# Kernel optimization log

Measured on AMD Instinct MI355X. Metric: run time of the kernel, lower is better.

The kernel has to match this reference:

```python
import jax, jax.numpy as jnp
import numpy as np

N = 50000      # nodes
E = 800000     # edges
CIN = 128
CH = 128
COUT = 64
EPS = 1e-5     # BatchNorm eps


def setup_inputs() -> dict:
    key = jax.random.key(0)
    ks = jax.random.split(key, 16)
    s = 0.1  # weight scale for numerical stability
    return {
        "x": jax.random.normal(ks[0], (N, CIN), jnp.float32),
        "edge_index": jax.random.randint(ks[1], (2, E), 0, N, jnp.int32),
        "edge_weights": jax.random.uniform(ks[2], (E,), jnp.float32),
        "w1": jax.random.normal(ks[3], (CIN, CH), jnp.float32) * s,
        "b1": jnp.zeros((CH,), jnp.float32),
        "bn1_g": jnp.ones((CH,), jnp.float32),
        "bn1_b": jnp.zeros((CH,), jnp.float32),
        "bn1_m": jax.random.normal(ks[4], (CH,), jnp.float32) * 0.1,
        "bn1_v": jax.random.uniform(ks[5], (CH,), jnp.float32) + 0.5,
        "conv_ws": jax.random.normal(ks[6], (2, CH, CH), jnp.float32) * s,
        "conv_bs": jnp.zeros((2, CH), jnp.float32),
        "bns_g": jnp.ones((2, CH), jnp.float32),
        "bns_b": jnp.zeros((2, CH), jnp.float32),
        "bns_m": jax.random.normal(ks[7], (2, CH), jnp.float32) * 0.1,
        "bns_v": jax.random.uniform(ks[8], (2, CH), jnp.float32) + 0.5,
        "lin1_w": jax.random.normal(ks[9], (CH, CH), jnp.float32) * s,
        "lin1_b": jnp.zeros((CH,), jnp.float32),
        "lin2_w": jax.random.normal(ks[10], (CH, COUT), jnp.float32) * s,
        "lin2_b": jnp.zeros((COUT,), jnp.float32),
    }


def _bn(h, g, b, m, v):
    # BatchNorm1d in eval mode: running statistics
    return (h - m) * jax.lax.rsqrt(v + EPS) * g + b


def _gcn(h, w, b, src, dst, norm, n):
    # GCNConv: out[dst] += norm_e * (h @ W)[src]  (self loops already in src/dst)
    h = h @ w
    msg = h[src] * norm[:, None]                 # [E+N, CH]
    return jax.ops.segment_sum(msg, dst, num_segments=n) + b


def reference(x, edge_index, edge_weights, w1, b1, bn1_g, bn1_b, bn1_m, bn1_v,
              conv_ws, conv_bs, bns_g, bns_b, bns_m, bns_v,
              lin1_w, lin1_b, lin2_w, lin2_b):
    n = x.shape[0]
    loop = jnp.arange(n, dtype=edge_index.dtype)
    src = jnp.concatenate([edge_index[0], loop])
    dst = jnp.concatenate([edge_index[1], loop])
    ew = jnp.concatenate([edge_weights, jnp.ones((n,), edge_weights.dtype)])
    # symmetric degree normalization (PyG gcn_norm)
    deg = jax.ops.segment_sum(ew, dst, num_segments=n)
    dis = jnp.where(deg > 0, jax.lax.rsqrt(deg), 0.0)
    norm = dis[src] * ew * dis[dst]

    lrelu = jax.nn.leaky_relu  # slope 0.01, matches F.leaky_relu default
    h = lrelu(_bn(_gcn(x, w1, b1, src, dst, norm, n), bn1_g, bn1_b, bn1_m, bn1_v))
    for i in range(conv_ws.shape[0]):
        h = lrelu(_bn(_gcn(h, conv_ws[i], conv_bs[i], src, dst, norm, n),
                      bns_g[i], bns_b[i], bns_m[i], bns_v[i]) + h)
    h = lrelu(h @ lin1_w + lin1_b)
    # dropout is identity in eval mode
    return h @ lin2_w + lin2_b
```

## Files before the change

kernel.cpp:

```cpp
#include <hip/hip_runtime.h>
#include <hip/hip_bf16.h>


constexpr int   NN    = 50000;
constexpr int   EE    = 800000;
constexpr int   CH    = 128;
constexpr int   SLOTS = 64;
constexpr int   NBUK  = 782;
constexpr int   RCAP  = 2048;
constexpr int   EPB   = 4096;
constexpr float EPS   = 1e-5f;

typedef __attribute__((ext_vector_type(8))) short bf16x8;
typedef __attribute__((ext_vector_type(4))) float f32x4;
typedef unsigned long long u64;
typedef unsigned short u16;

__device__ inline u16 f2bf_rne(float f) {
  unsigned u = __float_as_uint(f);
  unsigned r = u + 0x7fffu + ((u >> 16) & 1u);
  return (u16)(r >> 16);
}
__device__ inline float bf2f(unsigned h16) {
  return __uint_as_float(h16 << 16);
}


__global__ __launch_bounds__(256) void bin_kernel(const int* __restrict__ ei,
                                                  const float* __restrict__ ew,
                                                  unsigned* __restrict__ gcur,
                                                  u64* __restrict__ bins) {
  __shared__ unsigned cnt[NBUK];
  __shared__ unsigned base[NBUK];
  const int tid = threadIdx.x;
  for (int b = tid; b < NBUK; b += 256) cnt[b] = 0;
  __syncthreads();
  const int e0 = blockIdx.x * EPB;
  unsigned pk[16]; u16 bkt[16]; u16 rnk[16]; unsigned char dl[16];
  #pragma unroll
  for (int i = 0; i < 16; i++) {
    int e = e0 + i * 256 + tid;
    if (e < EE) {
      int s = ei[e], d = ei[EE + e];
      float w = ew[e];
      bkt[i] = (u16)(d >> 6);
      dl[i]  = (unsigned char)(d & 63);
      pk[i]  = ((unsigned)f2bf_rne(w) << 16) | (unsigned)s;
      rnk[i] = (u16)atomicAdd(&cnt[bkt[i]], 1u);
    } else bkt[i] = 0xffffu;
  }
  __syncthreads();
  for (int b = tid; b < NBUK; b += 256) {
    unsigned c = cnt[b];
    base[b] = c ? atomicAdd(&gcur[b * 16], c) : 0u;
  }
  __syncthreads();
  #pragma unroll
  for (int i = 0; i < 16; i++) {
    if (bkt[i] == 0xffffu) continue;
    unsigned pos = base[bkt[i]] + rnk[i];
    if (pos < RCAP)
      bins[(size_t)bkt[i] * RCAP + pos] = ((u64)dl[i] << 32) | pk[i];
  }
}


__global__ __launch_bounds__(256) void scatter_kernel(const unsigned* __restrict__ gcur,
                                                      const u64* __restrict__ bins,
                                                      unsigned* __restrict__ ell,
                                                      float* __restrict__ dis) {
  __shared__ unsigned rank[64];
  __shared__ float    wsum[64];
  const int b   = blockIdx.x;
  const int tid = threadIdx.x;
  if (tid < 64) { rank[tid] = 1u; wsum[tid] = 0.f; }
  __syncthreads();
  unsigned cnt = gcur[b * 16];
  if (cnt > RCAP) cnt = RCAP;
  const u64* src = bins + (size_t)b * RCAP;
  for (unsigned i = tid; i < cnt; i += 256) {
    u64 v = src[i];
    unsigned pk = (unsigned)v;
    unsigned dl = (unsigned)(v >> 32);
    unsigned r = atomicAdd(&rank[dl], 1u);
    if (r < SLOTS)
      ell[((size_t)(b * 64 + dl)) * SLOTS + r] = pk;
    atomicAdd(&wsum[dl], bf2f(pk >> 16));
  }
  __syncthreads();
  if (tid < 64) {
    int node = b * 64 + tid;
    if (node < NN) {
      unsigned c = rank[tid];
      if (c > SLOTS) c = SLOTS;
      ell[(size_t)node * SLOTS] = c;
      dis[node] = rsqrtf(1.0f + wsum[tid]);
    }
  }
}

constexpr int NB_WZ = (73728 + 384 + 255) / 256;

__global__ void wswz_kernel(
    const float* __restrict__ w1, const float* __restrict__ bn1_g, const float* __restrict__ bn1_v,
    const float* __restrict__ conv_ws, const float* __restrict__ bns_g, const float* __restrict__ bns_v,
    const float* __restrict__ lin1_w, const float* __restrict__ lin2_w,
    const float* __restrict__ b1, const float* __restrict__ bn1_b, const float* __restrict__ bn1_m,
    const float* __restrict__ conv_bs, const float* __restrict__ bns_b, const float* __restrict__ bns_m,
    u16* __restrict__ w1h, u16* __restrict__ w1l,
    u16* __restrict__ c0h, u16* __restrict__ c0l,
    u16* __restrict__ c1h, u16* __restrict__ c1l,
    u16* __restrict__ l1h, u16* __restrict__ l1l,
    u16* __restrict__ l2h, u16* __restrict__ l2l,
    float* __restrict__ beff)
{
  int idx = blockIdx.x * 256 + threadIdx.x;
  if (idx >= 73728) {
    int r = idx - 73728;
    if (r >= 384) return;
    int l = r >> 7, c = r & 127;
    float bc, gg, bb, mm, vv;
    if (l == 0) { bc = b1[c]; gg = bn1_g[c]; bb = bn1_b[c]; mm = bn1_m[c]; vv = bn1_v[c]; }
    else {
      int o = (l - 1) * 128 + c;
      bc = conv_bs[o]; gg = bns_g[o]; bb = bns_b[o]; mm = bns_m[o]; vv = bns_v[o];
    }
    beff[r] = (bc - mm) * gg * rsqrtf(vv + EPS) + bb;
    return;
  }
  const float* W; const float* g = nullptr; const float* v = nullptr;
  u16 *hi, *lo; int CO = 128; int local;
  if      (idx < 16384) { W = w1;              g = bn1_g;     v = bn1_v;     hi = w1h; lo = w1l; local = idx; }
  else if (idx < 32768) { W = conv_ws;         g = bns_g;     v = bns_v;     hi = c0h; lo = c0l; local = idx - 16384; }
  else if (idx < 49152) { W = conv_ws + 16384; g = bns_g+128; v = bns_v+128; hi = c1h; lo = c1l; local = idx - 32768; }
  else if (idx < 65536) { W = lin1_w;                                        hi = l1h; lo = l1l; local = idx - 49152; }
  else                  { W = lin2_w;                                        hi = l2h; lo = l2l; local = idx - 65536; CO = 64; }
  int k = local / CO, n = local % CO;
  float w = W[local];
  if (g) w *= g[n] * rsqrtf(v[n] + EPS);
  int NCT = CO / 16;
  int kchunk = k >> 5, kin = k & 31, quad = kin >> 3, j = kin & 7;
  int ct = n >> 4, l = (quad << 4) | (n & 15);
  size_t pos = ((size_t)(kchunk * NCT + ct) * 64 + l) * 8 + j;
  u16 h = f2bf_rne(w);
  hi[pos] = h;
  lo[pos] = f2bf_rne(w - bf2f(h));
}

template<int CO, int EPI, bool OUT_BF16, bool A_BF16, bool SCALE>
__global__ __launch_bounds__(256) void mgemm_kernel(
    const void* __restrict__ Ain,
    const u16* __restrict__ Whi, const u16* __restrict__ Wlo,
    const float* __restrict__ bias, const float* __restrict__ dis,
    void* __restrict__ Cout)
{
  constexpr int NCT = CO / 16;
  __shared__ float lds[64][CO + 4];

  const int tid  = threadIdx.x;
  const int wave = tid >> 6;
  const int lane = tid & 63;
  const int quad = lane >> 4;
  const int mrow = lane & 15;
  const int row0 = blockIdx.x * 64;

  int arow = row0 + wave * 16 + mrow;
  if (arow >= NN) arow = NN - 1;

  bf16x8 ahi[4], alo[4];
  if constexpr (A_BF16) {
    const u16* Ar = (const u16*)Ain + (size_t)arow * CH;
    #pragma unroll
    for (int c = 0; c < 4; c++)
      ahi[c] = *(const bf16x8*)(Ar + c * 32 + quad * 8);
  } else {
    const float* Ar = (const float*)Ain + (size_t)arow * CH;
    #pragma unroll
    for (int c = 0; c < 4; c++) {
      int off = c * 32 + quad * 8;
      float4 f0 = *(const float4*)(Ar + off);
      float4 f1 = *(const float4*)(Ar + off + 4);
      float f[8] = {f0.x, f0.y, f0.z, f0.w, f1.x, f1.y, f1.z, f1.w};
      #pragma unroll
      for (int j = 0; j < 8; j++) {
        u16 h = f2bf_rne(f[j]);
        ahi[c][j] = (short)h;
        alo[c][j] = (short)f2bf_rne(f[j] - bf2f(h));
      }
    }
  }

  f32x4 acc[NCT];
  #pragma unroll
  for (int t = 0; t < NCT; t++) acc[t] = (f32x4){0.f, 0.f, 0.f, 0.f};

  #pragma unroll
  for (int c = 0; c < 4; c++) {
    #pragma unroll
    for (int t = 0; t < NCT; t++) {
      size_t base = ((size_t)(c * NCT + t) * 64 + lane) * 8;
      bf16x8 bh = *(const bf16x8*)(Whi + base);
      bf16x8 bl = *(const bf16x8*)(Wlo + base);
      acc[t] = __builtin_amdgcn_mfma_f32_16x16x32_bf16(ahi[c], bh, acc[t], 0, 0, 0);
      if constexpr (!A_BF16)
        acc[t] = __builtin_amdgcn_mfma_f32_16x16x32_bf16(alo[c], bh, acc[t], 0, 0, 0);
      acc[t] = __builtin_amdgcn_mfma_f32_16x16x32_bf16(ahi[c], bl, acc[t], 0, 0, 0);
    }
  }

  #pragma unroll
  for (int t = 0; t < NCT; t++)
    #pragma unroll
    for (int r = 0; r < 4; r++)
      lds[wave * 16 + quad * 4 + r][t * 16 + mrow] = acc[t][r];
  __syncthreads();

  constexpr int TOTE = 64 * CO / 4;
  #pragma unroll
  for (int i = tid; i < TOTE; i += 256) {
    int row = (i * 4) / CO;
    int col = (i * 4) % CO;
    int grow = row0 + row;
    if (grow >= NN) continue;
    float rs = 1.0f;
    if constexpr (SCALE) rs = dis[grow];
    const float* lp = &lds[row][col];
    float o[4];
    #pragma unroll
    for (int q = 0; q < 4; q++) {
      float x = lp[q];
      if constexpr (EPI >= 1) {
        x += bias[col + q];
        if constexpr (EPI == 1) x = x > 0.f ? x : 0.01f * x;
      }
      if constexpr (SCALE) x *= rs;
      o[q] = x;
    }
    if constexpr (OUT_BF16) {
      u16* cp = (u16*)Cout + (size_t)grow * CO + col;
      unsigned p0 = ((unsigned)f2bf_rne(o[1]) << 16) | f2bf_rne(o[0]);
      unsigned p1 = ((unsigned)f2bf_rne(o[3]) << 16) | f2bf_rne(o[2]);
      *(uint2*)cp = make_uint2(p0, p1);
    } else {
      float* cp = (float*)Cout + (size_t)grow * CO + col;
      *(float4*)cp = make_float4(o[0], o[1], o[2], o[3]);
    }
  }
}

__global__ __launch_bounds__(256) void linf_kernel(
    const u16* __restrict__ Ain,
    const u16* __restrict__ l1h, const u16* __restrict__ l1l,
    const float* __restrict__ b1,
    const u16* __restrict__ l2h, const u16* __restrict__ l2l,
    const float* __restrict__ b2, float* __restrict__ out)
{
  __shared__ float lds[64][CH + 4];
  const int tid  = threadIdx.x;
  const int wave = tid >> 6;
  const int lane = tid & 63;
  const int quad = lane >> 4;
  const int mrow = lane & 15;
  const int row0 = blockIdx.x * 64;

  int arow = row0 + wave * 16 + mrow;
  if (arow >= NN) arow = NN - 1;

  bf16x8 a1[4];
  {
    const u16* Ar = Ain + (size_t)arow * CH;
    #pragma unroll
    for (int c = 0; c < 4; c++)
      a1[c] = *(const bf16x8*)(Ar + c * 32 + quad * 8);
  }
  f32x4 acc[8];
  #pragma unroll
  for (int t = 0; t < 8; t++) acc[t] = (f32x4){0.f, 0.f, 0.f, 0.f};
  #pragma unroll
  for (int c = 0; c < 4; c++) {
    #pragma unroll
    for (int t = 0; t < 8; t++) {
      size_t base = ((size_t)(c * 8 + t) * 64 + lane) * 8;
      bf16x8 bh = *(const bf16x8*)(l1h + base);
      bf16x8 bl = *(const bf16x8*)(l1l + base);
      acc[t] = __builtin_amdgcn_mfma_f32_16x16x32_bf16(a1[c], bh, acc[t], 0, 0, 0);
      acc[t] = __builtin_amdgcn_mfma_f32_16x16x32_bf16(a1[c], bl, acc[t], 0, 0, 0);
    }
  }
  #pragma unroll
  for (int t = 0; t < 8; t++) {
    float bb = b1[t * 16 + mrow];
    #pragma unroll
    for (int r = 0; r < 4; r++) {
      float x = acc[t][r] + bb;
      x = x > 0.f ? x : 0.01f * x;
      lds[wave * 16 + quad * 4 + r][t * 16 + mrow] = x;
    }
  }
  __syncthreads();

  f32x4 acc2[4];
  #pragma unroll
  for (int t = 0; t < 4; t++) acc2[t] = (f32x4){0.f, 0.f, 0.f, 0.f};
  const int lrow = wave * 16 + mrow;
  #pragma unroll
  for (int c = 0; c < 4; c++) {
    bf16x8 ahi, alo;
    const float* lp = &lds[lrow][c * 32 + quad * 8];
    float4 f0 = *(const float4*)lp;
    float4 f1 = *(const float4*)(lp + 4);
    float f[8] = {f0.x, f0.y, f0.z, f0.w, f1.x, f1.y, f1.z, f1.w};
    #pragma unroll
    for (int j = 0; j < 8; j++) {
      u16 h = f2bf_rne(f[j]);
      ahi[j] = (short)h;
      alo[j] = (short)f2bf_rne(f[j] - bf2f(h));
    }
    #pragma unroll
    for (int t = 0; t < 4; t++) {
      size_t base = ((size_t)(c * 4 + t) * 64 + lane) * 8;
      bf16x8 bh = *(const bf16x8*)(l2h + base);
      bf16x8 bl = *(const bf16x8*)(l2l + base);
      acc2[t] = __builtin_amdgcn_mfma_f32_16x16x32_bf16(ahi, bh, acc2[t], 0, 0, 0);
      acc2[t] = __builtin_amdgcn_mfma_f32_16x16x32_bf16(alo, bh, acc2[t], 0, 0, 0);
      acc2[t] = __builtin_amdgcn_mfma_f32_16x16x32_bf16(ahi, bl, acc2[t], 0, 0, 0);
    }
  }
  #pragma unroll
  for (int t = 0; t < 4; t++) {
    float bb = b2[t * 16 + mrow];
    #pragma unroll
    for (int r = 0; r < 4; r++) {
      int grow = row0 + wave * 16 + quad * 4 + r;
      if (grow < NN)
        out[(size_t)grow * 64 + t * 16 + mrow] = acc2[t][r] + bb;
    }
  }
}

template<bool RES>
__global__ __launch_bounds__(256) void agg_kernel(
    const u16* __restrict__ hw,
    const unsigned* __restrict__ ell, const float* __restrict__ dis,
    const float* __restrict__ beff,
    const u16* __restrict__ res, u16* __restrict__ out)
{
  int node = (blockIdx.x * blockDim.x + threadIdx.x) >> 6;
  int lane = threadIdx.x & 63;
  if (node >= NN) return;
  const int sub = lane & 15;
  const int grp = lane >> 4;

  unsigned myword = ell[(size_t)node * SLOTS + lane];
  int cnt = __shfl((int)myword, 0);
  if (cnt > SLOTS) cnt = SLOTS;

  float a[8] = {0.f, 0.f, 0.f, 0.f, 0.f, 0.f, 0.f, 0.f};

  for (int j = 0; j < cnt; j += 8) {
    int j0 = j + grp, j1 = j + 4 + grp;
    unsigned e0 = (unsigned)__shfl((int)myword, j0);
    unsigned e1 = (unsigned)__shfl((int)myword, j1 & 63);
    float    w0 = (j0 == 0) ? 1.0f : bf2f(e0 >> 16);
    unsigned s0 = (j0 == 0) ? (unsigned)node : (e0 & 0xffffu);
    float    w1 = bf2f(e1 >> 16);
    unsigned s1 = e1 & 0xffffu;
    if (j0 >= cnt) { w0 = 0.f; s0 = (unsigned)node; }
    if (j1 >= cnt) { w1 = 0.f; s1 = (unsigned)node; }
    uint4 h0 = *(const uint4*)(hw + (size_t)s0 * CH + sub * 8);
    uint4 h1 = *(const uint4*)(hw + (size_t)s1 * CH + sub * 8);
    a[0] = fmaf(w0, bf2f(h0.x & 0xffffu), a[0]); a[1] = fmaf(w0, bf2f(h0.x >> 16), a[1]);
    a[2] = fmaf(w0, bf2f(h0.y & 0xffffu), a[2]); a[3] = fmaf(w0, bf2f(h0.y >> 16), a[3]);
    a[4] = fmaf(w0, bf2f(h0.z & 0xffffu), a[4]); a[5] = fmaf(w0, bf2f(h0.z >> 16), a[5]);
    a[6] = fmaf(w0, bf2f(h0.w & 0xffffu), a[6]); a[7] = fmaf(w0, bf2f(h0.w >> 16), a[7]);
    a[0] = fmaf(w1, bf2f(h1.x & 0xffffu), a[0]); a[1] = fmaf(w1, bf2f(h1.x >> 16), a[1]);
    a[2] = fmaf(w1, bf2f(h1.y & 0xffffu), a[2]); a[3] = fmaf(w1, bf2f(h1.y >> 16), a[3]);
    a[4] = fmaf(w1, bf2f(h1.z & 0xffffu), a[4]); a[5] = fmaf(w1, bf2f(h1.z >> 16), a[5]);
    a[6] = fmaf(w1, bf2f(h1.w & 0xffffu), a[6]); a[7] = fmaf(w1, bf2f(h1.w >> 16), a[7]);
  }

  #pragma unroll
  for (int k = 0; k < 8; k++) {
    a[k] += __shfl_xor(a[k], 16);
    a[k] += __shfl_xor(a[k], 32);
  }

  if (grp == 0) {
    float disd = dis[node];
    int c = sub * 8;
    float4 be0 = *(const float4*)(beff + c);
    float4 be1 = *(const float4*)(beff + c + 4);
    float y[8];
    y[0] = a[0] * disd + be0.x; y[1] = a[1] * disd + be0.y;
    y[2] = a[2] * disd + be0.z; y[3] = a[3] * disd + be0.w;
    y[4] = a[4] * disd + be1.x; y[5] = a[5] * disd + be1.y;
    y[6] = a[6] * disd + be1.z; y[7] = a[7] * disd + be1.w;
    if constexpr (RES) {
      uint4 r = *(const uint4*)(res + (size_t)node * CH + c);
      y[0] += bf2f(r.x & 0xffffu); y[1] += bf2f(r.x >> 16);
      y[2] += bf2f(r.y & 0xffffu); y[3] += bf2f(r.y >> 16);
      y[4] += bf2f(r.z & 0xffffu); y[5] += bf2f(r.z >> 16);
      y[6] += bf2f(r.w & 0xffffu); y[7] += bf2f(r.w >> 16);
    }
    #pragma unroll
    for (int k = 0; k < 8; k++) y[k] = y[k] > 0.f ? y[k] : 0.01f * y[k];
    uint4 o;
    o.x = ((unsigned)f2bf_rne(y[1]) << 16) | f2bf_rne(y[0]);
    o.y = ((unsigned)f2bf_rne(y[3]) << 16) | f2bf_rne(y[2]);
    o.z = ((unsigned)f2bf_rne(y[5]) << 16) | f2bf_rne(y[4]);
    o.w = ((unsigned)f2bf_rne(y[7]) << 16) | f2bf_rne(y[6]);
    *(uint4*)(out + (size_t)node * CH + c) = o;
  }
}


extern "C" void kernel_launch(void* const* d_in, const int* in_sizes, int n_in,
                              void* d_out, int out_size, void* d_ws, size_t ws_size,
                              hipStream_t stream) {
  const float* x       = (const float*)d_in[0];
  const int*   ei      = (const int*)  d_in[1];
  const float* ew      = (const float*)d_in[2];
  const float* w1      = (const float*)d_in[3];
  const float* b1      = (const float*)d_in[4];
  const float* bn1_g   = (const float*)d_in[5];
  const float* bn1_b   = (const float*)d_in[6];
  const float* bn1_m   = (const float*)d_in[7];
  const float* bn1_v   = (const float*)d_in[8];
  const float* conv_ws = (const float*)d_in[9];
  const float* conv_bs = (const float*)d_in[10];
  const float* bns_g   = (const float*)d_in[11];
  const float* bns_b   = (const float*)d_in[12];
  const float* bns_m   = (const float*)d_in[13];
  const float* bns_v   = (const float*)d_in[14];
  const float* lin1_w  = (const float*)d_in[15];
  const float* lin1_b  = (const float*)d_in[16];
  const float* lin2_w  = (const float*)d_in[17];
  const float* lin2_b  = (const float*)d_in[18];
  float* out = (float*)d_out;

  size_t off = 0;
  auto alloc = [&](size_t elems) -> void* {
    void* p = (char*)d_ws + off * 4;
    off += (elems + 3) & ~(size_t)3;
    return p;
  };
  unsigned* gcur = (unsigned*)alloc(NBUK * 16);
  u64*      bins = (u64*)     alloc((size_t)NBUK * RCAP * 2);
  unsigned* ell  = (unsigned*)alloc((size_t)NN * SLOTS);
  float*    dis  = (float*)   alloc(NN);
  float*    beff = (float*)   alloc(3 * CH);
  u16*      hwb  = (u16*)     alloc((size_t)NN * CH / 2);
  u16*      hA   = (u16*)     alloc((size_t)NN * CH / 2);
  u16* w1h = (u16*)alloc(CH * CH / 2); u16* w1l = (u16*)alloc(CH * CH / 2);
  u16* c0h = (u16*)alloc(CH * CH / 2); u16* c0l = (u16*)alloc(CH * CH / 2);
  u16* c1h = (u16*)alloc(CH * CH / 2); u16* c1l = (u16*)alloc(CH * CH / 2);
  u16* l1h = (u16*)alloc(CH * CH / 2); u16* l1l = (u16*)alloc(CH * CH / 2);
  u16* l2h = (u16*)alloc(CH * 64 / 2); u16* l2l = (u16*)alloc(CH * 64 / 2);

  const int nb_bin  = (EE + EPB - 1) / EPB;
  const int nb_gemm = (NN + 63) / 64;
  const int nb_agg  = (NN * 64 + 255) / 256;
  dim3 B(256);

  hipMemsetAsync(gcur, 0, NBUK * 16 * sizeof(unsigned), stream);
  bin_kernel    <<<nb_bin, B, 0, stream>>>(ei, ew, gcur, bins);
  scatter_kernel<<<NBUK,   B, 0, stream>>>(gcur, bins, ell, dis);

  wswz_kernel<<<NB_WZ, B, 0, stream>>>(w1, bn1_g, bn1_v, conv_ws, bns_g, bns_v,
      lin1_w, lin2_w, b1, bn1_b, bn1_m, conv_bs, bns_b, bns_m,
      w1h, w1l, c0h, c0l, c1h, c1l, l1h, l1l, l2h, l2l, beff);

  mgemm_kernel<128, 0, true, false, true><<<nb_gemm, B, 0, stream>>>(x, w1h, w1l, nullptr, dis, hwb);
  agg_kernel<false><<<nb_agg, B, 0, stream>>>(hwb, ell, dis, beff, nullptr, hA);

  mgemm_kernel<128, 0, true, true, true><<<nb_gemm, B, 0, stream>>>(hA, c0h, c0l, nullptr, dis, hwb);
  agg_kernel<true><<<nb_agg, B, 0, stream>>>(hwb, ell, dis, beff + CH, hA, hA);

  mgemm_kernel<128, 0, true, true, true><<<nb_gemm, B, 0, stream>>>(hA, c1h, c1l, nullptr, dis, hwb);
  agg_kernel<true><<<nb_agg, B, 0, stream>>>(hwb, ell, dis, beff + 2 * CH, hA, hA);

  linf_kernel<<<nb_gemm, B, 0, stream>>>(hA, l1h, l1l, lin1_b, l2h, l2l, lin2_b, out);
}
```

Before: 324.3 us.

## Fuse GCN aggregation with the following layer's GEMM per 64-node block

```diff
diff --git a/kernel.cpp b/kernel.cpp
--- a/kernel.cpp
+++ b/kernel.cpp
@@ -147,16 +147,12 @@
   lo[pos] = f2bf_rne(w - bf2f(h));
 }
 
-template<int CO, int EPI, bool OUT_BF16, bool A_BF16, bool SCALE>
-__global__ __launch_bounds__(256) void mgemm_kernel(
-    const void* __restrict__ Ain,
+__global__ __launch_bounds__(256) void gemm1_kernel(
+    const float* __restrict__ Ain,
     const u16* __restrict__ Whi, const u16* __restrict__ Wlo,
-    const float* __restrict__ bias, const float* __restrict__ dis,
-    void* __restrict__ Cout)
+    const float* __restrict__ dis, u16* __restrict__ Cout)
 {
-  constexpr int NCT = CO / 16;
-  __shared__ float lds[64][CO + 4];
-
+  __shared__ float lds[64][CH + 4];
   const int tid  = threadIdx.x;
   const int wave = tid >> 6;
   const int lane = tid & 63;
@@ -168,88 +164,195 @@
   if (arow >= NN) arow = NN - 1;
 
   bf16x8 ahi[4], alo[4];
-  if constexpr (A_BF16) {
-    const u16* Ar = (const u16*)Ain + (size_t)arow * CH;
-    #pragma unroll
-    for (int c = 0; c < 4; c++)
-      ahi[c] = *(const bf16x8*)(Ar + c * 32 + quad * 8);
-  } else {
-    const float* Ar = (const float*)Ain + (size_t)arow * CH;
-    #pragma unroll
-    for (int c = 0; c < 4; c++) {
-      int off = c * 32 + quad * 8;
-      float4 f0 = *(const float4*)(Ar + off);
-      float4 f1 = *(const float4*)(Ar + off + 4);
-      float f[8] = {f0.x, f0.y, f0.z, f0.w, f1.x, f1.y, f1.z, f1.w};
-      #pragma unroll
-      for (int j = 0; j < 8; j++) {
-        u16 h = f2bf_rne(f[j]);
-        ahi[c][j] = (short)h;
-        alo[c][j] = (short)f2bf_rne(f[j] - bf2f(h));
-      }
-    }
-  }
-
-  f32x4 acc[NCT];
-  #pragma unroll
-  for (int t = 0; t < NCT; t++) acc[t] = (f32x4){0.f, 0.f, 0.f, 0.f};
-
+  const float* Ar = Ain + (size_t)arow * CH;
   #pragma unroll
   for (int c = 0; c < 4; c++) {
-    #pragma unroll
-    for (int t = 0; t < NCT; t++) {
-      size_t base = ((size_t)(c * NCT + t) * 64 + lane) * 8;
+    int off = c * 32 + quad * 8;
+    float4 f0 = *(const float4*)(Ar + off);
+    float4 f1 = *(const float4*)(Ar + off + 4);
+    float f[8] = {f0.x, f0.y, f0.z, f0.w, f1.x, f1.y, f1.z, f1.w};
+    #pragma unroll
+    for (int j = 0; j < 8; j++) {
+      u16 h = f2bf_rne(f[j]);
+      ahi[c][j] = (short)h;
+      alo[c][j] = (short)f2bf_rne(f[j] - bf2f(h));
+    }
+  }
+
+  f32x4 acc[8];
+  #pragma unroll
+  for (int t = 0; t < 8; t++) acc[t] = (f32x4){0.f, 0.f, 0.f, 0.f};
+  #pragma unroll
+  for (int c = 0; c < 4; c++) {
+    #pragma unroll
+    for (int t = 0; t < 8; t++) {
+      size_t base = ((size_t)(c * 8 + t) * 64 + lane) * 8;
       bf16x8 bh = *(const bf16x8*)(Whi + base);
       bf16x8 bl = *(const bf16x8*)(Wlo + base);
       acc[t] = __builtin_amdgcn_mfma_f32_16x16x32_bf16(ahi[c], bh, acc[t], 0, 0, 0);
-      if constexpr (!A_BF16)
-        acc[t] = __builtin_amdgcn_mfma_f32_16x16x32_bf16(alo[c], bh, acc[t], 0, 0, 0);
+      acc[t] = __builtin_amdgcn_mfma_f32_16x16x32_bf16(alo[c], bh, acc[t], 0, 0, 0);
       acc[t] = __builtin_amdgcn_mfma_f32_16x16x32_bf16(ahi[c], bl, acc[t], 0, 0, 0);
     }
   }
 
   #pragma unroll
-  for (int t = 0; t < NCT; t++)
+  for (int t = 0; t < 8; t++)
     #pragma unroll
     for (int r = 0; r < 4; r++)
       lds[wave * 16 + quad * 4 + r][t * 16 + mrow] = acc[t][r];
   __syncthreads();
 
-  constexpr int TOTE = 64 * CO / 4;
-  #pragma unroll
-  for (int i = tid; i < TOTE; i += 256) {
-    int row = (i * 4) / CO;
-    int col = (i * 4) % CO;
+  #pragma unroll
+  for (int i = tid; i < 64 * CH / 4; i += 256) {
+    int row = (i * 4) / CH;
+    int col = (i * 4) % CH;
     int grow = row0 + row;
     if (grow >= NN) continue;
-    float rs = 1.0f;
-    if constexpr (SCALE) rs = dis[grow];
+    float rs = dis[grow];
     const float* lp = &lds[row][col];
-    float o[4];
-    #pragma unroll
-    for (int q = 0; q < 4; q++) {
-      float x = lp[q];
-      if constexpr (EPI >= 1) {
-        x += bias[col + q];
-        if constexpr (EPI == 1) x = x > 0.f ? x : 0.01f * x;
+    u16* cp = (u16*)Cout + (size_t)grow * CH + col;
+    unsigned p0 = ((unsigned)f2bf_rne(lp[1] * rs) << 16) | f2bf_rne(lp[0] * rs);
+    unsigned p1 = ((unsigned)f2bf_rne(lp[3] * rs) << 16) | f2bf_rne(lp[2] * rs);
+    *(uint2*)cp = make_uint2(p0, p1);
+  }
+}
+
+template<bool RES>
+__global__ __launch_bounds__(256) void fuse_kernel(
+    const u16* __restrict__ hwin,
+    const unsigned* __restrict__ ell, const float* __restrict__ dis,
+    const float* __restrict__ beff, const u16* __restrict__ res,
+    const u16* __restrict__ Whi, const u16* __restrict__ Wlo,
+    u16* __restrict__ hout, u16* __restrict__ hwout)
+{
+  __shared__ float lds[64][CH + 4];
+  const int tid  = threadIdx.x;
+  const int wave = tid >> 6;
+  const int lane = tid & 63;
+  const int sub  = lane & 15;
+  const int grp  = lane >> 4;
+  const int row0 = blockIdx.x * 64;
+
+  for (int r = 0; r < 16; r++) {
+    int node = row0 + wave * 16 + r;
+    int nd = node < NN ? node : NN - 1;
+    unsigned myword = ell[(size_t)nd * SLOTS + lane];
+    int cnt = __shfl((int)myword, 0);
+    if (cnt > SLOTS) cnt = SLOTS;
+    float a[8] = {0.f, 0.f, 0.f, 0.f, 0.f, 0.f, 0.f, 0.f};
+    for (int j = 0; j < cnt; j += 8) {
+      int j0 = j + grp, j1 = j + 4 + grp;
+      unsigned e0 = (unsigned)__shfl((int)myword, j0 & 63);
+      unsigned e1 = (unsigned)__shfl((int)myword, j1 & 63);
+      float    w0 = (j0 == 0) ? 1.0f : bf2f(e0 >> 16);
+      unsigned s0 = (j0 == 0) ? (unsigned)nd : (e0 & 0xffffu);
+      float    w1 = bf2f(e1 >> 16);
+      unsigned s1 = e1 & 0xffffu;
+      if (j0 >= cnt) { w0 = 0.f; s0 = (unsigned)nd; }
+      if (j1 >= cnt) { w1 = 0.f; s1 = (unsigned)nd; }
+      uint4 h0 = *(const uint4*)(hwin + (size_t)s0 * CH + sub * 8);
+      uint4 h1 = *(const uint4*)(hwin + (size_t)s1 * CH + sub * 8);
+      a[0] = fmaf(w0, bf2f(h0.x & 0xffffu), a[0]); a[1] = fmaf(w0, bf2f(h0.x >> 16), a[1]);
+      a[2] = fmaf(w0, bf2f(h0.y & 0xffffu), a[2]); a[3] = fmaf(w0, bf2f(h0.y >> 16), a[3]);
+      a[4] = fmaf(w0, bf2f(h0.z & 0xffffu), a[4]); a[5] = fmaf(w0, bf2f(h0.z >> 16), a[5]);
+      a[6] = fmaf(w0, bf2f(h0.w & 0xffffu), a[6]); a[7] = fmaf(w0, bf2f(h0.w >> 16), a[7]);
+      a[0] = fmaf(w1, bf2f(h1.x & 0xffffu), a[0]); a[1] = fmaf(w1, bf2f(h1.x >> 16), a[1]);
+      a[2] = fmaf(w1, bf2f(h1.y & 0xffffu), a[2]); a[3] = fmaf(w1, bf2f(h1.y >> 16), a[3]);
+      a[4] = fmaf(w1, bf2f(h1.z & 0xffffu), a[4]); a[5] = fmaf(w1, bf2f(h1.z >> 16), a[5]);
+      a[6] = fmaf(w1, bf2f(h1.w & 0xffffu), a[6]); a[7] = fmaf(w1, bf2f(h1.w >> 16), a[7]);
+    }
+    #pragma unroll
+    for (int k = 0; k < 8; k++) {
+      a[k] += __shfl_xor(a[k], 16);
+      a[k] += __shfl_xor(a[k], 32);
+    }
+    if (grp == 0) {
+      float disd = dis[nd];
+      int c = sub * 8;
+      float4 be0 = *(const float4*)(beff + c);
+      float4 be1 = *(const float4*)(beff + c + 4);
+      float y[8];
+      y[0] = a[0] * disd + be0.x; y[1] = a[1] * disd + be0.y;
+      y[2] = a[2] * disd + be0.z; y[3] = a[3] * disd + be0.w;
+      y[4] = a[4] * disd + be1.x; y[5] = a[5] * disd + be1.y;
+      y[6] = a[6] * disd + be1.z; y[7] = a[7] * disd + be1.w;
+      if constexpr (RES) {
+        uint4 rr = *(const uint4*)(res + (size_t)nd * CH + c);
+        y[0] += bf2f(rr.x & 0xffffu); y[1] += bf2f(rr.x >> 16);
+        y[2] += bf2f(rr.y & 0xffffu); y[3] += bf2f(rr.y >> 16);
+        y[4] += bf2f(rr.z & 0xffffu); y[5] += bf2f(rr.z >> 16);
+        y[6] += bf2f(rr.w & 0xffffu); y[7] += bf2f(rr.w >> 16);
       }
-      if constexpr (SCALE) x *= rs;
-      o[q] = x;
-    }
-    if constexpr (OUT_BF16) {
-      u16* cp = (u16*)Cout + (size_t)grow * CO + col;
-      unsigned p0 = ((unsigned)f2bf_rne(o[1]) << 16) | f2bf_rne(o[0]);
-      unsigned p1 = ((unsigned)f2bf_rne(o[3]) << 16) | f2bf_rne(o[2]);
-      *(uint2*)cp = make_uint2(p0, p1);
-    } else {
-      float* cp = (float*)Cout + (size_t)grow * CO + col;
-      *(float4*)cp = make_float4(o[0], o[1], o[2], o[3]);
-    }
-  }
-}
-
-__global__ __launch_bounds__(256) void linf_kernel(
-    const u16* __restrict__ Ain,
+      #pragma unroll
+      for (int k = 0; k < 8; k++) y[k] = y[k] > 0.f ? y[k] : 0.01f * y[k];
+      uint4 o;
+      o.x = ((unsigned)f2bf_rne(y[1]) << 16) | f2bf_rne(y[0]);
+      o.y = ((unsigned)f2bf_rne(y[3]) << 16) | f2bf_rne(y[2]);
+      o.z = ((unsigned)f2bf_rne(y[5]) << 16) | f2bf_rne(y[4]);
+      o.w = ((unsigned)f2bf_rne(y[7]) << 16) | f2bf_rne(y[6]);
+      if (node < NN) *(uint4*)(hout + (size_t)node * CH + c) = o;
+      float* lp = &lds[wave * 16 + r][c];
+      lp[0] = bf2f(o.x & 0xffffu); lp[1] = bf2f(o.x >> 16);
+      lp[2] = bf2f(o.y & 0xffffu); lp[3] = bf2f(o.y >> 16);
+      lp[4] = bf2f(o.z & 0xffffu); lp[5] = bf2f(o.z >> 16);
+      lp[6] = bf2f(o.w & 0xffffu); lp[7] = bf2f(o.w >> 16);
+    }
+  }
+  __syncthreads();
+
+  bf16x8 af[4];
+  {
+    const float* hr = lds[wave * 16 + sub];
+    #pragma unroll
+    for (int c = 0; c < 4; c++) {
+      const float* p = hr + c * 32 + grp * 8;
+      #pragma unroll
+      for (int j = 0; j < 8; j++) af[c][j] = (short)f2bf_rne(p[j]);
+    }
+  }
+  __syncthreads();
+
+  f32x4 acc[8];
+  #pragma unroll
+  for (int t = 0; t < 8; t++) acc[t] = (f32x4){0.f, 0.f, 0.f, 0.f};
+  #pragma unroll
+  for (int c = 0; c < 4; c++) {
+    #pragma unroll
+    for (int t = 0; t < 8; t++) {
+      size_t base = ((size_t)(c * 8 + t) * 64 + lane) * 8;
+      bf16x8 bh = *(const bf16x8*)(Whi + base);
+      bf16x8 bl = *(const bf16x8*)(Wlo + base);
+      acc[t] = __builtin_amdgcn_mfma_f32_16x16x32_bf16(af[c], bh, acc[t], 0, 0, 0);
+      acc[t] = __builtin_amdgcn_mfma_f32_16x16x32_bf16(af[c], bl, acc[t], 0, 0, 0);
+    }
+  }
+
+  #pragma unroll
+  for (int t = 0; t < 8; t++)
+    #pragma unroll
+    for (int r = 0; r < 4; r++)
+      lds[wave * 16 + grp * 4 + r][t * 16 + sub] = acc[t][r];
+  __syncthreads();
+
+  #pragma unroll
+  for (int i = tid; i < 64 * CH / 4; i += 256) {
+    int row = (i * 4) / CH;
+    int col = (i * 4) % CH;
+    int grow = row0 + row;
+    if (grow >= NN) continue;
+    float rs = dis[grow];
+    const float* lp = &lds[row][col];
+    u16* cp = hwout + (size_t)grow * CH + col;
+    unsigned p0 = ((unsigned)f2bf_rne(lp[1] * rs) << 16) | f2bf_rne(lp[0] * rs);
+    unsigned p1 = ((unsigned)f2bf_rne(lp[3] * rs) << 16) | f2bf_rne(lp[2] * rs);
+    *(uint2*)cp = make_uint2(p0, p1);
+  }
+}
+
+__global__ __launch_bounds__(256) void fuse_last_kernel(
+    const u16* __restrict__ hwin,
+    const unsigned* __restrict__ ell, const float* __restrict__ dis,
+    const float* __restrict__ beff, const u16* __restrict__ res,
     const u16* __restrict__ l1h, const u16* __restrict__ l1l,
     const float* __restrict__ b1,
     const u16* __restrict__ l2h, const u16* __restrict__ l2l,
@@ -259,20 +362,80 @@
   const int tid  = threadIdx.x;
   const int wave = tid >> 6;
   const int lane = tid & 63;
-  const int quad = lane >> 4;
-  const int mrow = lane & 15;
+  const int sub  = lane & 15;
+  const int grp  = lane >> 4;
   const int row0 = blockIdx.x * 64;
 
-  int arow = row0 + wave * 16 + mrow;
-  if (arow >= NN) arow = NN - 1;
-
-  bf16x8 a1[4];
+  for (int r = 0; r < 16; r++) {
+    int node = row0 + wave * 16 + r;
+    int nd = node < NN ? node : NN - 1;
+    unsigned myword = ell[(size_t)nd * SLOTS + lane];
+    int cnt = __shfl((int)myword, 0);
+    if (cnt > SLOTS) cnt = SLOTS;
+    float a[8] = {0.f, 0.f, 0.f, 0.f, 0.f, 0.f, 0.f, 0.f};
+    for (int j = 0; j < cnt; j += 8) {
+      int j0 = j + grp, j1 = j + 4 + grp;
+      unsigned e0 = (unsigned)__shfl((int)myword, j0 & 63);
+      unsigned e1 = (unsigned)__shfl((int)myword, j1 & 63);
+      float    w0 = (j0 == 0) ? 1.0f : bf2f(e0 >> 16);
+      unsigned s0 = (j0 == 0) ? (unsigned)nd : (e0 & 0xffffu);
+      float    w1 = bf2f(e1 >> 16);
+      unsigned s1 = e1 & 0xffffu;
+      if (j0 >= cnt) { w0 = 0.f; s0 = (unsigned)nd; }
+      if (j1 >= cnt) { w1 = 0.f; s1 = (unsigned)nd; }
+      uint4 h0 = *(const uint4*)(hwin + (size_t)s0 * CH + sub * 8);
+      uint4 h1 = *(const uint4*)(hwin + (size_t)s1 * CH + sub * 8);
+      a[0] = fmaf(w0, bf2f(h0.x & 0xffffu), a[0]); a[1] = fmaf(w0, bf2f(h0.x >> 16), a[1]);
+      a[2] = fmaf(w0, bf2f(h0.y & 0xffffu), a[2]); a[3] = fmaf(w0, bf2f(h0.y >> 16), a[3]);
+      a[4] = fmaf(w0, bf2f(h0.z & 0xffffu), a[4]); a[5] = fmaf(w0, bf2f(h0.z >> 16), a[5]);
+      a[6] = fmaf(w0, bf2f(h0.w & 0xffffu), a[6]); a[7] = fmaf(w0, bf2f(h0.w >> 16), a[7]);
+      a[0] = fmaf(w1, bf2f(h1.x & 0xffffu), a[0]); a[1] = fmaf(w1, bf2f(h1.x >> 16), a[1]);
+      a[2] = fmaf(w1, bf2f(h1.y & 0xffffu), a[2]); a[3] = fmaf(w1, bf2f(h1.y >> 16), a[3]);
+      a[4] = fmaf(w1, bf2f(h1.z & 0xffffu), a[4]); a[5] = fmaf(w1, bf2f(h1.z >> 16), a[5]);
+      a[6] = fmaf(w1, bf2f(h1.w & 0xffffu), a[6]); a[7] = fmaf(w1, bf2f(h1.w >> 16), a[7]);
+    }
+    #pragma unroll
+    for (int k = 0; k < 8; k++) {
+      a[k] += __shfl_xor(a[k], 16);
+      a[k] += __shfl_xor(a[k], 32);
+    }
+    if (grp == 0) {
+      float disd = dis[nd];
+      int c = sub * 8;
+      float4 be0 = *(const float4*)(beff + c);
+      float4 be1 = *(const float4*)(beff + c + 4);
+      float y[8];
+      y[0] = a[0] * disd + be0.x; y[1] = a[1] * disd + be0.y;
+      y[2] = a[2] * disd + be0.z; y[3] = a[3] * disd + be0.w;
+      y[4] = a[4] * disd + be1.x; y[5] = a[5] * disd + be1.y;
+      y[6] = a[6] * disd + be1.z; y[7] = a[7] * disd + be1.w;
+      uint4 rr = *(const uint4*)(res + (size_t)nd * CH + c);
+      y[0] += bf2f(rr.x & 0xffffu); y[1] += bf2f(rr.x >> 16);
+      y[2] += bf2f(rr.y & 0xffffu); y[3] += bf2f(rr.y >> 16);
+      y[4] += bf2f(rr.z & 0xffffu); y[5] += bf2f(rr.z >> 16);
+      y[6] += bf2f(rr.w & 0xffffu); y[7] += bf2f(rr.w >> 16);
+      float* lp = &lds[wave * 16 + r][c];
+      #pragma unroll
+      for (int k = 0; k < 8; k++) {
+        float x = y[k] > 0.f ? y[k] : 0.01f * y[k];
+        lp[k] = bf2f(f2bf_rne(x));
+      }
+    }
+  }
+  __syncthreads();
+
+  bf16x8 af[4];
   {
-    const u16* Ar = Ain + (size_t)arow * CH;
-    #pragma unroll
-    for (int c = 0; c < 4; c++)
-      a1[c] = *(const bf16x8*)(Ar + c * 32 + quad * 8);
-  }
+    const float* hr = lds[wave * 16 + sub];
+    #pragma unroll
+    for (int c = 0; c < 4; c++) {
+      const float* p = hr + c * 32 + grp * 8;
+      #pragma unroll
+      for (int j = 0; j < 8; j++) af[c][j] = (short)f2bf_rne(p[j]);
+    }
+  }
+  __syncthreads();
+
   f32x4 acc[8];
   #pragma unroll
   for (int t = 0; t < 8; t++) acc[t] = (f32x4){0.f, 0.f, 0.f, 0.f};
@@ -283,18 +446,18 @@
       size_t base = ((size_t)(c * 8 + t) * 64 + lane) * 8;
       bf16x8 bh = *(const bf16x8*)(l1h + base);
       bf16x8 bl = *(const bf16x8*)(l1l + base);
-      acc[t] = __builtin_amdgcn_mfma_f32_16x16x32_bf16(a1[c], bh, acc[t], 0, 0, 0);
-      acc[t] = __builtin_amdgcn_mfma_f32_16x16x32_bf16(a1[c], bl, acc[t], 0, 0, 0);
+      acc[t] = __builtin_amdgcn_mfma_f32_16x16x32_bf16(af[c], bh, acc[t], 0, 0, 0);
+      acc[t] = __builtin_amdgcn_mfma_f32_16x16x32_bf16(af[c], bl, acc[t], 0, 0, 0);
     }
   }
   #pragma unroll
   for (int t = 0; t < 8; t++) {
-    float bb = b1[t * 16 + mrow];
+    float bb = b1[t * 16 + sub];
     #pragma unroll
     for (int r = 0; r < 4; r++) {
       float x = acc[t][r] + bb;
       x = x > 0.f ? x : 0.01f * x;
-      lds[wave * 16 + quad * 4 + r][t * 16 + mrow] = x;
+      lds[wave * 16 + grp * 4 + r][t * 16 + sub] = x;
     }
   }
   __syncthreads();
@@ -302,11 +465,11 @@
   f32x4 acc2[4];
   #pragma unroll
   for (int t = 0; t < 4; t++) acc2[t] = (f32x4){0.f, 0.f, 0.f, 0.f};
-  const int lrow = wave * 16 + mrow;
+  const int lrow = wave * 16 + sub;
   #pragma unroll
   for (int c = 0; c < 4; c++) {
     bf16x8 ahi, alo;
-    const float* lp = &lds[lrow][c * 32 + quad * 8];
+    const float* lp = &lds[lrow][c * 32 + grp * 8];
     float4 f0 = *(const float4*)lp;
     float4 f1 = *(const float4*)(lp + 4);
     float f[8] = {f0.x, f0.y, f0.z, f0.w, f1.x, f1.y, f1.z, f1.w};
@@ -328,88 +491,13 @@
   }
   #pragma unroll
   for (int t = 0; t < 4; t++) {
-    float bb = b2[t * 16 + mrow];
+    float bb = b2[t * 16 + sub];
     #pragma unroll
     for (int r = 0; r < 4; r++) {
-      int grow = row0 + wave * 16 + quad * 4 + r;
+      int grow = row0 + wave * 16 + grp * 4 + r;
       if (grow < NN)
-        out[(size_t)grow * 64 + t * 16 + mrow] = acc2[t][r] + bb;
-    }
-  }
-}
-
-template<bool RES>
-__global__ __launch_bounds__(256) void agg_kernel(
-    const u16* __restrict__ hw,
-    const unsigned* __restrict__ ell, const float* __restrict__ dis,
-    const float* __restrict__ beff,
-    const u16* __restrict__ res, u16* __restrict__ out)
-{
-  int node = (blockIdx.x * blockDim.x + threadIdx.x) >> 6;
-  int lane = threadIdx.x & 63;
-  if (node >= NN) return;
-  const int sub = lane & 15;
-  const int grp = lane >> 4;
-
-  unsigned myword = ell[(size_t)node * SLOTS + lane];
-  int cnt = __shfl((int)myword, 0);
-  if (cnt > SLOTS) cnt = SLOTS;
-
-  float a[8] = {0.f, 0.f, 0.f, 0.f, 0.f, 0.f, 0.f, 0.f};
-
-  for (int j = 0; j < cnt; j += 8) {
-    int j0 = j + grp, j1 = j + 4 + grp;
-    unsigned e0 = (unsigned)__shfl((int)myword, j0);
-    unsigned e1 = (unsigned)__shfl((int)myword, j1 & 63);
-    float    w0 = (j0 == 0) ? 1.0f : bf2f(e0 >> 16);
-    unsigned s0 = (j0 == 0) ? (unsigned)node : (e0 & 0xffffu);
-    float    w1 = bf2f(e1 >> 16);
-    unsigned s1 = e1 & 0xffffu;
-    if (j0 >= cnt) { w0 = 0.f; s0 = (unsigned)node; }
-    if (j1 >= cnt) { w1 = 0.f; s1 = (unsigned)node; }
-    uint4 h0 = *(const uint4*)(hw + (size_t)s0 * CH + sub * 8);
-    uint4 h1 = *(const uint4*)(hw + (size_t)s1 * CH + sub * 8);
-    a[0] = fmaf(w0, bf2f(h0.x & 0xffffu), a[0]); a[1] = fmaf(w0, bf2f(h0.x >> 16), a[1]);
-    a[2] = fmaf(w0, bf2f(h0.y & 0xffffu), a[2]); a[3] = fmaf(w0, bf2f(h0.y >> 16), a[3]);
-    a[4] = fmaf(w0, bf2f(h0.z & 0xffffu), a[4]); a[5] = fmaf(w0, bf2f(h0.z >> 16), a[5]);
-    a[6] = fmaf(w0, bf2f(h0.w & 0xffffu), a[6]); a[7] = fmaf(w0, bf2f(h0.w >> 16), a[7]);
-    a[0] = fmaf(w1, bf2f(h1.x & 0xffffu), a[0]); a[1] = fmaf(w1, bf2f(h1.x >> 16), a[1]);
-    a[2] = fmaf(w1, bf2f(h1.y & 0xffffu), a[2]); a[3] = fmaf(w1, bf2f(h1.y >> 16), a[3]);
-    a[4] = fmaf(w1, bf2f(h1.z & 0xffffu), a[4]); a[5] = fmaf(w1, bf2f(h1.z >> 16), a[5]);
-    a[6] = fmaf(w1, bf2f(h1.w & 0xffffu), a[6]); a[7] = fmaf(w1, bf2f(h1.w >> 16), a[7]);
-  }
-
-  #pragma unroll
-  for (int k = 0; k < 8; k++) {
-    a[k] += __shfl_xor(a[k], 16);
-    a[k] += __shfl_xor(a[k], 32);
-  }
-
-  if (grp == 0) {
-    float disd = dis[node];
-    int c = sub * 8;
-    float4 be0 = *(const float4*)(beff + c);
-    float4 be1 = *(const float4*)(beff + c + 4);
-    float y[8];
-    y[0] = a[0] * disd + be0.x; y[1] = a[1] * disd + be0.y;
-    y[2] = a[2] * disd + be0.z; y[3] = a[3] * disd + be0.w;
-    y[4] = a[4] * disd + be1.x; y[5] = a[5] * disd + be1.y;
-    y[6] = a[6] * disd + be1.z; y[7] = a[7] * disd + be1.w;
-    if constexpr (RES) {
-      uint4 r = *(const uint4*)(res + (size_t)node * CH + c);
-      y[0] += bf2f(r.x & 0xffffu); y[1] += bf2f(r.x >> 16);
-      y[2] += bf2f(r.y & 0xffffu); y[3] += bf2f(r.y >> 16);
-      y[4] += bf2f(r.z & 0xffffu); y[5] += bf2f(r.z >> 16);
-      y[6] += bf2f(r.w & 0xffffu); y[7] += bf2f(r.w >> 16);
-    }
-    #pragma unroll
-    for (int k = 0; k < 8; k++) y[k] = y[k] > 0.f ? y[k] : 0.01f * y[k];
-    uint4 o;
-    o.x = ((unsigned)f2bf_rne(y[1]) << 16) | f2bf_rne(y[0]);
-    o.y = ((unsigned)f2bf_rne(y[3]) << 16) | f2bf_rne(y[2]);
-    o.z = ((unsigned)f2bf_rne(y[5]) << 16) | f2bf_rne(y[4]);
-    o.w = ((unsigned)f2bf_rne(y[7]) << 16) | f2bf_rne(y[6]);
-    *(uint4*)(out + (size_t)node * CH + c) = o;
+        out[(size_t)grow * 64 + t * 16 + sub] = acc2[t][r] + bb;
+    }
   }
 }
 
@@ -449,8 +537,10 @@
   unsigned* ell  = (unsigned*)alloc((size_t)NN * SLOTS);
   float*    dis  = (float*)   alloc(NN);
   float*    beff = (float*)   alloc(3 * CH);
+  u16*      hwa  = (u16*)     alloc((size_t)NN * CH / 2);
   u16*      hwb  = (u16*)     alloc((size_t)NN * CH / 2);
-  u16*      hA   = (u16*)     alloc((size_t)NN * CH / 2);
+  u16*      h1   = (u16*)     alloc((size_t)NN * CH / 2);
+  u16*      h2   = (u16*)     alloc((size_t)NN * CH / 2);
   u16* w1h = (u16*)alloc(CH * CH / 2); u16* w1l = (u16*)alloc(CH * CH / 2);
   u16* c0h = (u16*)alloc(CH * CH / 2); u16* c0l = (u16*)alloc(CH * CH / 2);
   u16* c1h = (u16*)alloc(CH * CH / 2); u16* c1l = (u16*)alloc(CH * CH / 2);
@@ -459,7 +549,6 @@
 
   const int nb_bin  = (EE + EPB - 1) / EPB;
   const int nb_gemm = (NN + 63) / 64;
-  const int nb_agg  = (NN * 64 + 255) / 256;
   dim3 B(256);
 
   hipMemsetAsync(gcur, 0, NBUK * 16 * sizeof(unsigned), stream);
@@ -470,14 +559,14 @@
       lin1_w, lin2_w, b1, bn1_b, bn1_m, conv_bs, bns_b, bns_m,
       w1h, w1l, c0h, c0l, c1h, c1l, l1h, l1l, l2h, l2l, beff);
 
-  mgemm_kernel<128, 0, true, false, true><<<nb_gemm, B, 0, stream>>>(x, w1h, w1l, nullptr, dis, hwb);
-  agg_kernel<false><<<nb_agg, B, 0, stream>>>(hwb, ell, dis, beff, nullptr, hA);
-
-  mgemm_kernel<128, 0, true, true, true><<<nb_gemm, B, 0, stream>>>(hA, c0h, c0l, nullptr, dis, hwb);
-  agg_kernel<true><<<nb_agg, B, 0, stream>>>(hwb, ell, dis, beff + CH, hA, hA);
-
-  mgemm_kernel<128, 0, true, true, true><<<nb_gemm, B, 0, stream>>>(hA, c1h, c1l, nullptr, dis, hwb);
-  agg_kernel<true><<<nb_agg, B, 0, stream>>>(hwb, ell, dis, beff + 2 * CH, hA, hA);
-
-  linf_kernel<<<nb_gemm, B, 0, stream>>>(hA, l1h, l1l, lin1_b, l2h, l2l, lin2_b, out);
-}
+  gemm1_kernel<<<nb_gemm, B, 0, stream>>>(x, w1h, w1l, dis, hwa);
+
+  fuse_kernel<false><<<nb_gemm, B, 0, stream>>>(hwa, ell, dis, beff, nullptr,
+      c0h, c0l, h1, hwb);
+
+  fuse_kernel<true><<<nb_gemm, B, 0, stream>>>(hwb, ell, dis, beff + CH, h1,
+      c1h, c1l, h2, hwa);
+
+  fuse_last_kernel<<<nb_gemm, B, 0, stream>>>(hwa, ell, dis, beff + 2 * CH, h2,
+      l1h, l1l, lin1_b, l2h, l2l, lin2_b, out);
+}
```

Result: faster. 315.2 us (-2.8%).
